# Kernel optimization log

Measured on AMD Instinct MI355X. Metric: run time of the kernel, lower is better.

Reference implementation:

```python
import jax, jax.numpy as jnp
import numpy as np

B, C, O, H, W = 8, 64, 64, 128, 128


def conv3x3(x, w, b):
    # x: [B,Cin,H,W], w: [Cout,Cin,3,3], stride 1, padding 1
    y = jax.lax.conv_general_dilated(
        x, w, window_strides=(1, 1), padding=((1, 1), (1, 1)),
        dimension_numbers=("NCHW", "OIHW", "NCHW"))
    return y + b[None, :, None, None]


def setup_inputs() -> dict:
    key = jax.random.key(0)
    ks = jax.random.split(key, 6)
    fan = C * 9
    x = jax.random.normal(ks[0], (B, C, H, W), dtype=jnp.float32)
    w_main = jax.random.normal(ks[1], (O, C, 3, 3), dtype=jnp.float32) / np.sqrt(fan)
    # small offset weights keep sampled locations near the regular grid (realistic post-training regime)
    w_offset = jax.random.normal(ks[2], (18, C, 3, 3), dtype=jnp.float32) * 0.05 / np.sqrt(fan)
    b_offset = jnp.zeros((18,), dtype=jnp.float32)
    w_mask = jax.random.normal(ks[3], (9, C, 3, 3), dtype=jnp.float32) / np.sqrt(fan)
    b_mask = jnp.zeros((9,), dtype=jnp.float32)
    return {"x": x, "w_main": w_main, "w_offset": w_offset,
            "b_offset": b_offset, "w_mask": w_mask, "b_mask": b_mask}


def deform_conv2d(x, w_main, offset, mask):
    # torchvision.ops.deform_conv2d: kernel 3x3, stride 1, pad 1, dilation 1, no bias
    Bb, Cc, Hh, Ww = x.shape
    Oo = w_main.shape[0]
    off = offset.reshape(Bb, 9, 2, Hh, Ww)
    dy, dx = off[:, :, 0], off[:, :, 1]            # [B,9,H,W]; pairs ordered (y,x), k row-major
    k = jnp.arange(9)
    kh = (k // 3 - 1).astype(x.dtype)              # kernel row offset in {-1,0,1}
    kw = (k % 3 - 1).astype(x.dtype)
    iy = jnp.arange(Hh, dtype=x.dtype)
    ix = jnp.arange(Ww, dtype=x.dtype)
    # sampling positions p = p0 + p_k + delta_p
    py = dy + iy[None, None, :, None] + kh[None, :, None, None]
    px = dx + ix[None, None, None, :] + kw[None, :, None, None]

    y0 = jnp.floor(py)
    x0 = jnp.floor(px)
    ly = py - y0
    lx = px - x0
    y0i = y0.astype(jnp.int32)
    x0i = x0.astype(jnp.int32)
    y1i = y0i + 1
    x1i = x0i + 1

    bidx = jnp.arange(Bb)[:, None, None, None]

    def corner(yi, xi, wgt):
        # zero-padding semantics: out-of-bounds neighbors contribute 0
        valid = (yi >= 0) & (yi < Hh) & (xi >= 0) & (xi < Ww)
        v = x[bidx, :, jnp.clip(yi, 0, Hh - 1), jnp.clip(xi, 0, Ww - 1)]  # [B,9,H,W,C]
        return v * (wgt * valid)[..., None]

    samp = (corner(y0i, x0i, (1 - ly) * (1 - lx))
            + corner(y0i, x1i, (1 - ly) * lx)
            + corner(y1i, x0i, ly * (1 - lx))
            + corner(y1i, x1i, ly * lx))
    samp = samp * mask[..., None]                  # modulation mask (dcn v2)
    # contract sampled patches with weights: [B,9,H,W,C] x [O,C,9] -> [B,O,H,W]
    return jnp.einsum("bkhwc,ock->bohw", samp, w_main.reshape(Oo, Cc, 9))


def reference(x, w_main, w_offset, b_offset, w_mask, b_mask):
    offset = conv3x3(x, w_offset, b_offset)                 # [B,18,H,W]
    mask = jax.nn.sigmoid(conv3x3(x, w_mask, b_mask))       # [B,9,H,W]
    return deform_conv2d(x, w_main, offset, mask)
```

## Files before the change

kernel.cpp:

```cpp
#include <hip/hip_runtime.h>
#include <math.h>

#define BB 8
#define CC 64
#define OO 64
#define HH 128
#define WW 128
#define HW (HH*WW)
#define NPIX (BB*HW)

typedef __bf16 bf16x8 __attribute__((ext_vector_type(8)));
typedef float floatx4 __attribute__((ext_vector_type(4)));
typedef float f32x2 __attribute__((ext_vector_type(2)));
typedef unsigned short ushort_t;

#define XT_BYTES  16777216
#define OM_BYTES  14680064
#define WT_BYTES  73728

__device__ __forceinline__ unsigned short f2b(float f) {
    unsigned u = __float_as_uint(f);
    u += 0x7fffu + ((u >> 16) & 1u);
    return (unsigned short)(u >> 16);
}

__device__ __forceinline__ unsigned cvt_pk_bf16(float lo, float hi) {
    unsigned r;
    asm("v_cvt_pk_bf16_f32 %0, %1, %2" : "=v"(r) : "v"(lo), "v"(hi));
    return r;
}

__device__ __forceinline__ f32x2 pk_fma(f32x2 a, f32x2 b, f32x2 c) {
    f32x2 d;
    asm("v_pk_fma_f32 %0, %1, %2, %3" : "=v"(d) : "v"(a), "v"(b), "v"(c));
    return d;
}

__device__ __forceinline__ f32x2 pk_mul(f32x2 a, f32x2 b) {
    f32x2 d;
    asm("v_pk_mul_f32 %0, %1, %2" : "=v"(d) : "v"(a), "v"(b));
    return d;
}

__global__ __launch_bounds__(256) void transpose_kernel(
    const float* __restrict__ x, ushort_t* __restrict__ xt)
{
    __shared__ float tile[64][33];
    int bh = blockIdx.x;
    int w0 = blockIdx.y * 32;
    int b  = bh >> 7;
    int h  = bh & 127;
    int t  = threadIdx.x;
    int tx = t & 31;
    int ty = t >> 5;

    #pragma unroll
    for (int j = 0; j < 8; ++j) {
        int c = ty * 8 + j;
        tile[c][tx] = x[(((size_t)(b*CC + c))*HH + h)*WW + (w0 + tx)];
    }
    __syncthreads();
    #pragma unroll
    for (int j = 0; j < 4; ++j) {
        int w  = ty + 8*j;
        int cp = tx;
        unsigned u = cvt_pk_bf16(tile[2*cp][w], tile[2*cp+1][w]);
        *(unsigned*)(xt + (((size_t)(b*HH + h))*WW + (w0 + w))*CC + 2*cp) = u;
    }
}

__global__ __launch_bounds__(256) void repack_kernel(
    const float* __restrict__ wm, const float* __restrict__ woff,
    const float* __restrict__ wmask, ushort_t* __restrict__ wt,
    ushort_t* __restrict__ wb)
{
    int i = blockIdx.x * 256 + threadIdx.x;
    if (i < 36864) {
        int o = i / 576, k = i % 576, tap = k >> 6, c = k & 63;
        wt[i] = f2b(wm[o*576 + c*9 + tap]);
    }
    int j = i - 36864;
    if (j >= 0 && j < 18432) {
        int o = j / 576, k = j % 576, tap = k >> 6, c = k & 63;
        float v = 0.f;
        if (o < 18)      v = woff[o*576 + c*9 + tap];
        else if (o < 27) v = wmask[(o-18)*576 + c*9 + tap];
        wb[j] = f2b(v);
    }
}

__global__ __launch_bounds__(256) void conv27_kernel(
    const ushort_t* __restrict__ xt, const ushort_t* __restrict__ wb,
    const float* __restrict__ boff, const float* __restrict__ bmsk,
    float* __restrict__ om)
{
    __shared__ ushort_t win[18*18*72];
    int bid = blockIdx.x;
    int b  = bid >> 6;
    int th = (bid >> 3) & 7;
    int tw = bid & 7;
    int h0 = th * 16, w0 = tw * 16;
    int t = threadIdx.x;

    for (int idx = t; idx < 18*18*8; idx += 256) {
        int r   = idx / 144;
        int rem = idx - r*144;
        int col = rem >> 3;
        int ch  = (rem & 7) << 3;
        int y = h0 + r - 1, x = w0 + col - 1;
        uint4 val = make_uint4(0,0,0,0);
        if ((unsigned)y < (unsigned)HH && (unsigned)x < (unsigned)WW)
            val = *(const uint4*)(xt + ((((size_t)b*HH + y)*WW + x) << 6) + ch);
        *(uint4*)(win + (r*18 + col)*72 + ch) = val;
    }
    __syncthreads();

    int lane = t & 63, wv = t >> 6;
    int n = lane & 15, quad = lane >> 4;
    const ushort_t* wb0 = wb + n*576;
    const ushort_t* wb1 = wb + (16 + n)*576;

    floatx4 acc0[4], acc1[4];
    #pragma unroll
    for (int mt = 0; mt < 4; ++mt) {
        acc0[mt] = (floatx4){0.f,0.f,0.f,0.f};
        acc1[mt] = (floatx4){0.f,0.f,0.f,0.f};
    }

    #pragma unroll
    for (int s = 0; s < 18; ++s) {
        int tap  = s >> 1;
        int tr   = tap / 3, tc = tap % 3;
        int coff = (s & 1)*32 + quad*8;
        int kk = tap*64 + coff;
        bf16x8 b0 = *(const bf16x8*)(wb0 + kk);
        bf16x8 b1 = *(const bf16x8*)(wb1 + kk);
        #pragma unroll
        for (int mt = 0; mt < 4; ++mt) {
            int ty = wv*4 + mt;
            bf16x8 a = *(const bf16x8*)(win + ((ty + tr)*18 + (n + tc))*72 + coff);
            acc0[mt] = __builtin_amdgcn_mfma_f32_16x16x32_bf16(a, b0, acc0[mt], 0, 0, 0);
            acc1[mt] = __builtin_amdgcn_mfma_f32_16x16x32_bf16(a, b1, acc1[mt], 0, 0, 0);
        }
    }

    #pragma unroll
    for (int mt = 0; mt < 4; ++mt) {
        int ty = wv*4 + mt;
        #pragma unroll
        for (int r = 0; r < 4; ++r) {
            int tx = quad*4 + r;
            size_t p = ((size_t)(b*HH + h0 + ty))*WW + (w0 + tx);
            float* dst = om + p*28;
            dst[n] = acc0[mt][r] + boff[n];
            int o1 = 16 + n;
            if (o1 < 18) {
                dst[o1] = acc1[mt][r] + boff[o1];
            } else if (o1 < 27) {
                float z = acc1[mt][r] + bmsk[o1 - 18];
                dst[o1] = 1.f / (1.f + expf(-z));
            } else if (o1 == 27) {
                dst[27] = 0.f;
            }
        }
    }
}

__global__ __launch_bounds__(256, 4) void deform_kernel(
    const ushort_t* __restrict__ xt, const float* __restrict__ om,
    const ushort_t* __restrict__ wt, float* __restrict__ out)
{
    __shared__ ushort_t samp[2*64*72];

    int t = threadIdx.x;
    int lane = t & 63, wv = t >> 6;
    int bid = blockIdx.x;
    int b  = bid >> 8;
    int th = (bid >> 4) & 15;
    int tw = bid & 15;
    int h0 = th * 8, w0 = tw * 8;

    int pa = t >> 2, cg = t & 3;
    int ph = pa >> 3, pw = pa & 7;
    int h_a = h0 + ph, w_a = w0 + pw;
    const float* omp = om + (((size_t)(b*HH + h_a))*WW + w_a) * 28;
    const ushort_t* xbase = xt + ((size_t)b << 20);

    int n = lane & 15, quad = lane >> 4;
    floatx4 acc[4];
    #pragma unroll
    for (int i = 0; i < 4; ++i) acc[i] = (floatx4){0.f,0.f,0.f,0.f};
    const ushort_t* wrow = wt + (wv*16 + n)*576;

    float dy = omp[0], dx = omp[1], m = omp[18];

    for (int k = 0; k < 9; ++k) {
        ushort_t* sb = samp + (k & 1) * (64*72);

        float dy_n = 0.f, dx_n = 0.f, m_n = 0.f;
        if (k < 8) { dy_n = omp[2*k + 2]; dx_n = omp[2*k + 3]; m_n = omp[19 + k]; }

        int kr = k / 3, kc = k - kr*3;
        float py = (float)(h_a + kr - 1) + dy;
        float px = (float)(w_a + kc - 1) + dx;
        float y0f = floorf(py), x0f = floorf(px);
        float ly = py - y0f, lx = px - x0f;
        int y0 = (int)y0f, x0 = (int)x0f, y1 = y0 + 1, x1 = x0 + 1;
        float vy0 = ((unsigned)y0 < (unsigned)HH) ? 1.f : 0.f;
        float vy1 = ((unsigned)y1 < (unsigned)HH) ? 1.f : 0.f;
        float vx0 = ((unsigned)x0 < (unsigned)WW) ? 1.f : 0.f;
        float vx1 = ((unsigned)x1 < (unsigned)WW) ? 1.f : 0.f;

        float cw[4] = { (1.f-ly)*(1.f-lx)*vy0*vx0*m,
                        (1.f-ly)*lx      *vy0*vx1*m,
                        ly*(1.f-lx)      *vy1*vx0*m,
                        ly*lx            *vy1*vx1*m };
        int ys[4] = { y0, y0, y1, y1 };
        int xs[4] = { x0, x1, x0, x1 };

        dy = dy_n; dx = dx_n; m = m_n;

        uint4 q[8];
        #pragma unroll
        for (int cn = 0; cn < 4; ++cn) {
            int yc = min(max(ys[cn], 0), HH-1);
            int xc = min(max(xs[cn], 0), WW-1);
            const uint4* cp = (const uint4*)(xbase + (((yc << 7) + xc) << 6) + cg*16);
            q[2*cn]   = cp[0];
            q[2*cn+1] = cp[1];
        }

        f32x2 v2[8];
        {
            f32x2 w2; w2.x = cw[0]; w2.y = cw[0];
            unsigned u0[8] = { q[0].x, q[0].y, q[0].z, q[0].w,
                               q[1].x, q[1].y, q[1].z, q[1].w };
            #pragma unroll
            for (int j = 0; j < 8; ++j) {
                f32x2 f;
                f.x = __uint_as_float(u0[j] << 16);
                f.y = __uint_as_float(u0[j] & 0xffff0000u);
                v2[j] = pk_mul(f, w2);
            }
        }
        #pragma unroll
        for (int cn = 1; cn < 4; ++cn) {
            f32x2 w2; w2.x = cw[cn]; w2.y = cw[cn];
            unsigned u0[8] = { q[2*cn].x, q[2*cn].y, q[2*cn].z, q[2*cn].w,
                               q[2*cn+1].x, q[2*cn+1].y, q[2*cn+1].z, q[2*cn+1].w };
            #pragma unroll
            for (int j = 0; j < 8; ++j) {
                f32x2 f;
                f.x = __uint_as_float(u0[j] << 16);
                f.y = __uint_as_float(u0[j] & 0xffff0000u);
                v2[j] = pk_fma(f, w2, v2[j]);
            }
        }

        {
            unsigned uu[8];
            #pragma unroll
            for (int j = 0; j < 8; ++j)
                uu[j] = cvt_pk_bf16(v2[j].x, v2[j].y);
            uint4* dst = (uint4*)(sb + pa*72 + cg*16);
            dst[0] = make_uint4(uu[0], uu[1], uu[2], uu[3]);
            dst[1] = make_uint4(uu[4], uu[5], uu[6], uu[7]);
        }
        __syncthreads();

        #pragma unroll
        for (int half = 0; half < 2; ++half) {
            bf16x8 bfrag = *(const bf16x8*)(wrow + k*64 + half*32 + quad*8);
            #pragma unroll
            for (int mt = 0; mt < 4; ++mt) {
                bf16x8 afrag = *(const bf16x8*)(sb + (mt*16 + n)*72 + half*32 + quad*8);
                acc[mt] = __builtin_amdgcn_mfma_f32_16x16x32_bf16(afrag, bfrag, acc[mt], 0, 0, 0);
            }
        }
    }

    float* op = out + ((size_t)b*OO + (wv*16 + n))*HW;
    #pragma unroll
    for (int mt = 0; mt < 4; ++mt) {
        int row = h0 + mt*2 + (quad >> 1);
        int col = w0 + (quad & 1)*4;
        float4 st = make_float4(acc[mt][0], acc[mt][1], acc[mt][2], acc[mt][3]);
        *(float4*)(op + row*WW + col) = st;
    }
}

extern "C" void kernel_launch(void* const* d_in, const int* in_sizes, int n_in,
                              void* d_out, int out_size, void* d_ws, size_t ws_size,
                              hipStream_t stream)
{
    const float* x      = (const float*)d_in[0];
    const float* w_main = (const float*)d_in[1];
    const float* w_off  = (const float*)d_in[2];
    const float* b_off  = (const float*)d_in[3];
    const float* w_msk  = (const float*)d_in[4];
    const float* b_msk  = (const float*)d_in[5];
    float* out = (float*)d_out;

    unsigned char* ws = (unsigned char*)d_ws;
    ushort_t* xt = (ushort_t*)ws;
    float*    om = (float*)(ws + XT_BYTES);
    ushort_t* wt = (ushort_t*)(ws + XT_BYTES + OM_BYTES);
    ushort_t* wb = (ushort_t*)(ws + XT_BYTES + OM_BYTES + WT_BYTES);

    dim3 tgrid(BB*HH, WW/32);
    transpose_kernel<<<tgrid, 256, 0, stream>>>(x, xt);

    repack_kernel<<<(36864 + 18432 + 255)/256, 256, 0, stream>>>(
        w_main, w_off, w_msk, wt, wb);

    conv27_kernel<<<NPIX/256, 256, 0, stream>>>(xt, wb, b_off, b_msk, om);

    deform_kernel<<<NPIX/64, 256, 0, stream>>>(xt, om, wt, out);
}
```

Before: 161.2 us.

## Make each wave own its pixels to remove block-wide barrier in deform kernel

Work is split so that each wave samples its own 16 pixels into a private double-buffered LDS region and computes all 64 output channels for them, rather than sharing 64 sampled pixels across the four waves by output-channel group. This removes the per-tap __syncthreads, since the wave that writes the samples is the one that reads them. In exchange, every wave now loads all four weight fragments per half from global/L2 instead of one. Intra-wave LDS visibility is assumed without an explicit wave barrier, and output stores now go to four channel planes per wave.

```diff
diff --git a/kernel.cpp b/kernel.cpp
--- a/kernel.cpp
+++ b/kernel.cpp
@@ -170,7 +170,7 @@
     const ushort_t* __restrict__ xt, const float* __restrict__ om,
     const ushort_t* __restrict__ wt, float* __restrict__ out)
 {
-    __shared__ ushort_t samp[2*64*72];
+    __shared__ ushort_t samp[4*2*16*72];
 
     int t = threadIdx.x;
     int lane = t & 63, wv = t >> 6;
@@ -180,9 +180,9 @@
     int tw = bid & 15;
     int h0 = th * 8, w0 = tw * 8;
 
-    int pa = t >> 2, cg = t & 3;
-    int ph = pa >> 3, pw = pa & 7;
-    int h_a = h0 + ph, w_a = w0 + pw;
+    int px_s = lane >> 2, cg = lane & 3;
+    int p_lin = wv*16 + px_s;
+    int h_a = h0 + (p_lin >> 3), w_a = w0 + (p_lin & 7);
     const float* omp = om + (((size_t)(b*HH + h_a))*WW + w_a) * 28;
     const ushort_t* xbase = xt + ((size_t)b << 20);
 
@@ -190,12 +190,13 @@
     floatx4 acc[4];
     #pragma unroll
     for (int i = 0; i < 4; ++i) acc[i] = (floatx4){0.f,0.f,0.f,0.f};
-    const ushort_t* wrow = wt + (wv*16 + n)*576;
+
+    ushort_t* wbuf = samp + wv * (2*16*72);
 
     float dy = omp[0], dx = omp[1], m = omp[18];
 
     for (int k = 0; k < 9; ++k) {
-        ushort_t* sb = samp + (k & 1) * (64*72);
+        ushort_t* sb = wbuf + (k & 1) * (16*72);
 
         float dy_n = 0.f, dx_n = 0.f, m_n = 0.f;
         if (k < 8) { dy_n = omp[2*k + 2]; dx_n = omp[2*k + 3]; m_n = omp[19 + k]; }
@@ -262,29 +263,30 @@
             #pragma unroll
             for (int j = 0; j < 8; ++j)
                 uu[j] = cvt_pk_bf16(v2[j].x, v2[j].y);
-            uint4* dst = (uint4*)(sb + pa*72 + cg*16);
+            uint4* dst = (uint4*)(sb + px_s*72 + cg*16);
             dst[0] = make_uint4(uu[0], uu[1], uu[2], uu[3]);
             dst[1] = make_uint4(uu[4], uu[5], uu[6], uu[7]);
         }
-        __syncthreads();
 
         #pragma unroll
         for (int half = 0; half < 2; ++half) {
-            bf16x8 bfrag = *(const bf16x8*)(wrow + k*64 + half*32 + quad*8);
+            bf16x8 afrag = *(const bf16x8*)(sb + n*72 + half*32 + quad*8);
             #pragma unroll
-            for (int mt = 0; mt < 4; ++mt) {
-                bf16x8 afrag = *(const bf16x8*)(sb + (mt*16 + n)*72 + half*32 + quad*8);
-                acc[mt] = __builtin_amdgcn_mfma_f32_16x16x32_bf16(afrag, bfrag, acc[mt], 0, 0, 0);
+            for (int og = 0; og < 4; ++og) {
+                bf16x8 bfrag = *(const bf16x8*)(wt + (og*16 + n)*576
+                                                + k*64 + half*32 + quad*8);
+                acc[og] = __builtin_amdgcn_mfma_f32_16x16x32_bf16(
+                              afrag, bfrag, acc[og], 0, 0, 0);
             }
         }
     }
 
-    float* op = out + ((size_t)b*OO + (wv*16 + n))*HW;
-    #pragma unroll
-    for (int mt = 0; mt < 4; ++mt) {
-        int row = h0 + mt*2 + (quad >> 1);
-        int col = w0 + (quad & 1)*4;
-        float4 st = make_float4(acc[mt][0], acc[mt][1], acc[mt][2], acc[mt][3]);
+    int row = h0 + wv*2 + (quad >> 1);
+    int col = w0 + (quad & 1)*4;
+    #pragma unroll
+    for (int og = 0; og < 4; ++og) {
+        float* op = out + ((size_t)b*OO + (og*16 + n))*HW;
+        float4 st = make_float4(acc[og][0], acc[og][1], acc[og][2], acc[og][3]);
         *(float4*)(op + row*WW + col) = st;
     }
 }
```

New measurement: 205.3 us. +27.4%, slower.

## Batch three kernel taps per LDS stage to cut barriers in deform kernel

Applied to the files above, without the earlier changes.

The deform kernel now gathers and interpolates three kernel taps (one kernel row) into a wider shared buffer before each barrier, rather than one tap per double-buffered stage. This drops the barrier count from nine to five and lets each wave issue more MFMAs per barrier. Weight fragments for the three taps are preloaded into registers per row. In exchange it loses double buffering, so there is a barrier after the MFMAs, and it uses more LDS and registers, with occupancy lowered to three blocks per CU.

```diff
diff --git a/kernel.cpp b/kernel.cpp
--- a/kernel.cpp
+++ b/kernel.cpp
@@ -166,11 +166,13 @@
     }
 }
 
-__global__ __launch_bounds__(256, 4) void deform_kernel(
+#define SROW 200
+
+__global__ __launch_bounds__(256, 3) void deform_kernel(
     const ushort_t* __restrict__ xt, const float* __restrict__ om,
     const ushort_t* __restrict__ wt, float* __restrict__ out)
 {
-    __shared__ ushort_t samp[2*64*72];
+    __shared__ ushort_t samp[64*SROW];
 
     int t = threadIdx.x;
     int lane = t & 63, wv = t >> 6;
@@ -190,91 +192,120 @@
     floatx4 acc[4];
     #pragma unroll
     for (int i = 0; i < 4; ++i) acc[i] = (floatx4){0.f,0.f,0.f,0.f};
-    const ushort_t* wrow = wt + (wv*16 + n)*576;
-
-    float dy = omp[0], dx = omp[1], m = omp[18];
-
-    for (int k = 0; k < 9; ++k) {
-        ushort_t* sb = samp + (k & 1) * (64*72);
-
-        float dy_n = 0.f, dx_n = 0.f, m_n = 0.f;
-        if (k < 8) { dy_n = omp[2*k + 2]; dx_n = omp[2*k + 3]; m_n = omp[19 + k]; }
-
-        int kr = k / 3, kc = k - kr*3;
-        float py = (float)(h_a + kr - 1) + dy;
-        float px = (float)(w_a + kc - 1) + dx;
-        float y0f = floorf(py), x0f = floorf(px);
-        float ly = py - y0f, lx = px - x0f;
-        int y0 = (int)y0f, x0 = (int)x0f, y1 = y0 + 1, x1 = x0 + 1;
-        float vy0 = ((unsigned)y0 < (unsigned)HH) ? 1.f : 0.f;
-        float vy1 = ((unsigned)y1 < (unsigned)HH) ? 1.f : 0.f;
-        float vx0 = ((unsigned)x0 < (unsigned)WW) ? 1.f : 0.f;
-        float vx1 = ((unsigned)x1 < (unsigned)WW) ? 1.f : 0.f;
-
-        float cw[4] = { (1.f-ly)*(1.f-lx)*vy0*vx0*m,
-                        (1.f-ly)*lx      *vy0*vx1*m,
-                        ly*(1.f-lx)      *vy1*vx0*m,
-                        ly*lx            *vy1*vx1*m };
-        int ys[4] = { y0, y0, y1, y1 };
-        int xs[4] = { x0, x1, x0, x1 };
-
-        dy = dy_n; dx = dx_n; m = m_n;
-
-        uint4 q[8];
-        #pragma unroll
-        for (int cn = 0; cn < 4; ++cn) {
-            int yc = min(max(ys[cn], 0), HH-1);
-            int xc = min(max(xs[cn], 0), WW-1);
-            const uint4* cp = (const uint4*)(xbase + (((yc << 7) + xc) << 6) + cg*16);
-            q[2*cn]   = cp[0];
-            q[2*cn+1] = cp[1];
-        }
-
-        f32x2 v2[8];
-        {
-            f32x2 w2; w2.x = cw[0]; w2.y = cw[0];
-            unsigned u0[8] = { q[0].x, q[0].y, q[0].z, q[0].w,
-                               q[1].x, q[1].y, q[1].z, q[1].w };
-            #pragma unroll
-            for (int j = 0; j < 8; ++j) {
-                f32x2 f;
-                f.x = __uint_as_float(u0[j] << 16);
-                f.y = __uint_as_float(u0[j] & 0xffff0000u);
-                v2[j] = pk_mul(f, w2);
-            }
-        }
-        #pragma unroll
-        for (int cn = 1; cn < 4; ++cn) {
-            f32x2 w2; w2.x = cw[cn]; w2.y = cw[cn];
-            unsigned u0[8] = { q[2*cn].x, q[2*cn].y, q[2*cn].z, q[2*cn].w,
-                               q[2*cn+1].x, q[2*cn+1].y, q[2*cn+1].z, q[2*cn+1].w };
-            #pragma unroll
-            for (int j = 0; j < 8; ++j) {
-                f32x2 f;
-                f.x = __uint_as_float(u0[j] << 16);
-                f.y = __uint_as_float(u0[j] & 0xffff0000u);
-                v2[j] = pk_fma(f, w2, v2[j]);
-            }
-        }
-
-        {
-            unsigned uu[8];
-            #pragma unroll
-            for (int j = 0; j < 8; ++j)
-                uu[j] = cvt_pk_bf16(v2[j].x, v2[j].y);
-            uint4* dst = (uint4*)(sb + pa*72 + cg*16);
-            dst[0] = make_uint4(uu[0], uu[1], uu[2], uu[3]);
-            dst[1] = make_uint4(uu[4], uu[5], uu[6], uu[7]);
-        }
+    const ushort_t* wrow = wt + (wv*16 + n)*576 + quad*8;
+
+    float dyv[3], dxv[3], mv[3];
+    #pragma unroll
+    for (int j = 0; j < 3; ++j) {
+        dyv[j] = omp[2*j]; dxv[j] = omp[2*j+1]; mv[j] = omp[18+j];
+    }
+
+    #pragma unroll
+    for (int p = 0; p < 3; ++p) {
+        bf16x8 wf[6];
+        #pragma unroll
+        for (int s = 0; s < 6; ++s)
+            wf[s] = *(const bf16x8*)(wrow + (p*6 + s)*32);
+
+        #pragma unroll
+        for (int kk = 0; kk < 3; ++kk) {
+            float py = (float)(h_a + p  - 1) + dyv[kk];
+            float px = (float)(w_a + kk - 1) + dxv[kk];
+            float y0f = floorf(py), x0f = floorf(px);
+            float ly = py - y0f, lx = px - x0f;
+            int y0 = (int)y0f, x0 = (int)x0f, y1 = y0 + 1, x1 = x0 + 1;
+            float vy0 = ((unsigned)y0 < (unsigned)HH) ? 1.f : 0.f;
+            float vy1 = ((unsigned)y1 < (unsigned)HH) ? 1.f : 0.f;
+            float vx0 = ((unsigned)x0 < (unsigned)WW) ? 1.f : 0.f;
+            float vx1 = ((unsigned)x1 < (unsigned)WW) ? 1.f : 0.f;
+            float m   = mv[kk];
+
+            float cw[4] = { (1.f-ly)*(1.f-lx)*vy0*vx0*m,
+                            (1.f-ly)*lx      *vy0*vx1*m,
+                            ly*(1.f-lx)      *vy1*vx0*m,
+                            ly*lx            *vy1*vx1*m };
+            int ys[4] = { y0, y0, y1, y1 };
+            int xs[4] = { x0, x1, x0, x1 };
+
+            uint4 q[8];
+            #pragma unroll
+            for (int cn = 0; cn < 4; ++cn) {
+                int yc = min(max(ys[cn], 0), HH-1);
+                int xc = min(max(xs[cn], 0), WW-1);
+                const uint4* cp = (const uint4*)(xbase + (((yc << 7) + xc) << 6) + cg*16);
+                q[2*cn]   = cp[0];
+                q[2*cn+1] = cp[1];
+            }
+
+            f32x2 v2[8];
+            {
+                f32x2 w2; w2.x = cw[0]; w2.y = cw[0];
+                unsigned u0[8] = { q[0].x, q[0].y, q[0].z, q[0].w,
+                                   q[1].x, q[1].y, q[1].z, q[1].w };
+                #pragma unroll
+                for (int j = 0; j < 8; ++j) {
+                    f32x2 f;
+                    f.x = __uint_as_float(u0[j] << 16);
+                    f.y = __uint_as_float(u0[j] & 0xffff0000u);
+                    v2[j] = pk_mul(f, w2);
+                }
+            }
+            #pragma unroll
+            for (int cn = 1; cn < 4; ++cn) {
+                f32x2 w2; w2.x = cw[cn]; w2.y = cw[cn];
+                unsigned u0[8] = { q[2*cn].x, q[2*cn].y, q[2*cn].z, q[2*cn].w,
+                                   q[2*cn+1].x, q[2*cn+1].y, q[2*cn+1].z, q[2*cn+1].w };
+                #pragma unroll
+                for (int j = 0; j < 8; ++j) {
+                    f32x2 f;
+                    f.x = __uint_as_float(u0[j] << 16);
+                    f.y = __uint_as_float(u0[j] & 0xffff0000u);
+                    v2[j] = pk_fma(f, w2, v2[j]);
+                }
+            }
+
+            {
+                unsigned uu[8];
+                #pragma unroll
+                for (int j = 0; j < 8; ++j)
+                    uu[j] = cvt_pk_bf16(v2[j].x, v2[j].y);
+                uint4* dst = (uint4*)(samp + pa*SROW + kk*64 + cg*16);
+                dst[0] = make_uint4(uu[0], uu[1], uu[2], uu[3]);
+                dst[1] = make_uint4(uu[4], uu[5], uu[6], uu[7]);
+            }
+        }
+
+        float dyn_[3], dxn_[3], mn_[3];
+        if (p < 2) {
+            #pragma unroll
+            for (int j = 0; j < 3; ++j) {
+                int k2 = 3*(p+1) + j;
+                dyn_[j] = omp[2*k2]; dxn_[j] = omp[2*k2+1]; mn_[j] = omp[18+k2];
+            }
+        }
+
         __syncthreads();
 
         #pragma unroll
-        for (int half = 0; half < 2; ++half) {
-            bf16x8 bfrag = *(const bf16x8*)(wrow + k*64 + half*32 + quad*8);
-            #pragma unroll
-            for (int mt = 0; mt < 4; ++mt) {
-                bf16x8 afrag = *(const bf16x8*)(sb + (mt*16 + n)*72 + half*32 + quad*8);
-                acc[mt] = __builtin_amdgcn_mfma_f32_16x16x32_bf16(afrag, bfrag, acc[mt], 0, 0, 0);
+        for (int kk = 0; kk < 3; ++kk) {
+            #pragma unroll
+            for (int half = 0; half < 2; ++half) {
+                bf16x8 bfrag = wf[kk*2 + half];
+                #pragma unroll
+                for (int mt = 0; mt < 4; ++mt) {
+                    bf16x8 afrag = *(const bf16x8*)(samp + (mt*16 + n)*SROW
+                                                    + kk*64 + half*32 + quad*8);
+                    acc[mt] = __builtin_amdgcn_mfma_f32_16x16x32_bf16(
+                                  afrag, bfrag, acc[mt], 0, 0, 0);
+                }
+            }
+        }
+
+        if (p < 2) {
+            __syncthreads();
+            #pragma unroll
+            for (int j = 0; j < 3; ++j) {
+                dyv[j] = dyn_[j]; dxv[j] = dxn_[j]; mv[j] = mn_[j];
             }
         }
     }
```

Result: faster. 157.7 us (-2.2%).
